# Kernel optimization log

Measured on AMD Instinct MI355X. Metric: run time of the kernel, lower is better.

## Reference

```python
import jax, jax.numpy as jnp
import numpy as np

B, TAU, T0V, D, PD, RD, DO, K = 2048, 32, 96, 64, 3, 1, 64, 16
R = 1.0  # radius for radius_graph


def setup_inputs() -> dict:
    key = jax.random.key(0)
    ks = jax.random.split(key, 9)
    return {
        "x": jax.random.normal(ks[0], (B, TAU, D), jnp.float32),
        "pos": jax.random.uniform(ks[1], (B, TAU, PD), jnp.float32),
        "rot": jax.random.uniform(ks[2], (B, TAU, RD), jnp.float32),
        "old_x": jax.random.normal(ks[3], (B, 128, D), jnp.float32),
        "old_pos": jax.random.uniform(ks[4], (B, 128, PD), jnp.float32),
        "old_rot": jax.random.uniform(ks[5], (B, 128, RD), jnp.float32),
        "W_self": jax.random.normal(ks[6], (D + PD + RD, DO), jnp.float32) * 0.1,
        "W_nbr": jax.random.normal(ks[7], (D + PD + RD, DO), jnp.float32) * 0.1,
        "bias": jax.random.normal(ks[8], (DO,), jnp.float32) * 0.1,
        "T0": T0V,
        "tau": TAU,
    }


def reference(x, pos, rot, old_x, old_pos, old_rot, W_self, W_nbr, bias, T0, tau):
    # --- update(): scatter new observations into the state buffers ---
    # (regular case: T[b]=T0, taus[b]=tau for all b, so new_idx is a static slice)
    new_x = old_x.at[:, T0:T0 + tau].set(x)
    new_pos = old_pos.at[:, T0:T0 + tau].set(pos)
    new_rot = old_rot.at[:, T0:T0 + tau].set(rot)

    L = T0 + tau  # valid (non-padded) nodes per env
    nx, npv, nr = new_x[:, :L], new_pos[:, :L], new_rot[:, :L]
    h = jnp.concatenate([nx, npv, nr], axis=-1)  # [B, L, D+PD+RD] node features

    # --- radius_graph(r, max_num_neighbors=K, loop=True) + remove_noncausal_edges ---
    # edge (j -> i) kept iff ||pos_j - pos_i|| <= r and j < i (causal, drops self-loops)
    diff = npv[:, :, None, :] - npv[:, None, :, :]           # [B, L, L, PD]
    d2 = jnp.sum(diff * diff, axis=-1)                        # [B, L, L] (target i, source j)
    t_idx = jnp.arange(L)
    causal = t_idx[None, :] < t_idx[:, None]                  # [L, L] j < i
    mask = causal[None, :, :] & (d2 <= R * R)
    masked_d2 = jnp.where(mask, d2, jnp.inf)
    neg_d, nbr_idx = jax.lax.top_k(-masked_d2, K)             # k nearest causal in-radius
    valid = jnp.isfinite(neg_d)                               # [B, L, K]

    # --- gnn(): one message-passing layer (stand-in for external gnn) ---
    msg = h @ W_nbr                                           # [B, L, DO]
    gathered = jax.vmap(lambda m, i: m[i])(msg, nbr_idx)      # [B, L, K, DO]
    agg = jnp.sum(gathered * valid[..., None].astype(msg.dtype), axis=2)
    out = jax.nn.relu(h @ W_self + agg + bias)                # [B, L, DO]

    # --- gather flat_new_idx / scatter into padded output ---
    padded_output = out[:, T0:T0 + tau]                       # [B, tau, DO]
    return padded_output, new_x, new_pos, new_rot
```

## Files before the change

kernel.cpp:

```cpp
#include <hip/hip_runtime.h>
#include <hip/hip_bf16.h>
#include <cstdint>
#include <cstddef>

#define NB 2048
#define TAU 32
#define T0C 96
#define LQ 128
#define DD 64
#define DOUT 64
#define KK 16
#define INVK 0xFFFFFFFFu

typedef unsigned int u32;
typedef __attribute__((ext_vector_type(8))) short short8;
typedef __attribute__((ext_vector_type(4))) float f32x4;

__device__ __forceinline__ float fmul_exact(float a, float b) {
  float r; asm("v_mul_f32 %0, %1, %2" : "=v"(r) : "v"(a), "v"(b)); return r;
}
__device__ __forceinline__ float fadd_exact(float a, float b) {
  float r; asm("v_add_f32 %0, %1, %2" : "=v"(r) : "v"(a), "v"(b)); return r;
}
__device__ __forceinline__ unsigned short f2bf(float f) {
  __hip_bfloat16 h = __float2bfloat16(f);
  return *reinterpret_cast<unsigned short*>(&h);
}
__device__ __forceinline__ u32 shfl_xor_u32(u32 v, int mask) {
  return (u32)__shfl_xor((int)v, mask, 64);
}

__device__ __forceinline__ void barrier_lgkm() {
  asm volatile("s_waitcnt lgkmcnt(0)" ::: "memory");
  __builtin_amdgcn_s_barrier();
  __builtin_amdgcn_sched_barrier(0);
}

#define CA(i, j) { u32 _lo = min(kd[i], kd[j]); u32 _hi = max(kd[i], kd[j]); kd[i] = _lo; kd[j] = _hi; }
#define CD(i, j) { u32 _lo = min(kd[i], kd[j]); u32 _hi = max(kd[i], kd[j]); kd[i] = _hi; kd[j] = _lo; }

#define SORT16() do { \
  CA(0,1)  CD(2,3)  CA(4,5)  CD(6,7)  CA(8,9)  CD(10,11) CA(12,13) CD(14,15) \
  CA(0,2)  CA(1,3)  CD(4,6)  CD(5,7)  CA(8,10) CA(9,11)  CD(12,14) CD(13,15) \
  CA(0,1)  CA(2,3)  CD(4,5)  CD(6,7)  CA(8,9)  CA(10,11) CD(12,13) CD(14,15) \
  CA(0,4)  CA(1,5)  CA(2,6)  CA(3,7)  CD(8,12) CD(9,13)  CD(10,14) CD(11,15) \
  CA(0,2)  CA(1,3)  CA(4,6)  CA(5,7)  CD(8,10) CD(9,11)  CD(12,14) CD(13,15) \
  CA(0,1)  CA(2,3)  CA(4,5)  CA(6,7)  CD(8,9)  CD(10,11) CD(12,13) CD(14,15) \
  CA(0,8)  CA(1,9)  CA(2,10) CA(3,11) CA(4,12) CA(5,13)  CA(6,14)  CA(7,15)  \
  CA(0,4)  CA(1,5)  CA(2,6)  CA(3,7)  CA(8,12) CA(9,13)  CA(10,14) CA(11,15) \
  CA(0,2)  CA(1,3)  CA(4,6)  CA(5,7)  CA(8,10) CA(9,11)  CA(12,14) CA(13,15) \
  CA(0,1)  CA(2,3)  CA(4,5)  CA(6,7)  CA(8,9)  CA(10,11) CA(12,13) CA(14,15) \
} while (0)

#define MERGE16() do { \
  CA(0,8)  CA(1,9)  CA(2,10) CA(3,11) CA(4,12) CA(5,13)  CA(6,14)  CA(7,15)  \
  CA(0,4)  CA(1,5)  CA(2,6)  CA(3,7)  CA(8,12) CA(9,13)  CA(10,14) CA(11,15) \
  CA(0,2)  CA(1,3)  CA(4,6)  CA(5,7)  CA(8,10) CA(9,11)  CA(12,14) CA(13,15) \
  CA(0,1)  CA(2,3)  CA(4,5)  CA(6,7)  CA(8,9)  CA(10,11) CA(12,13) CA(14,15) \
} while (0)

#define SHUF_MERGE(mask) do { \
  u32 pb[16]; \
  _Pragma("unroll") \
  for (int _i = 0; _i < 16; ++_i) pb[_i] = shfl_xor_u32(kd[15 - _i], mask); \
  _Pragma("unroll") \
  for (int _i = 0; _i < 16; ++_i) kd[_i] = min(kd[_i], pb[_i]); \
  MERGE16(); \
} while (0)

__global__ __launch_bounds__(256) void prep_w(
    const float* __restrict__ W_nbr, const float* __restrict__ W_self,
    unsigned short* __restrict__ wst) {
  int idx = blockIdx.x * 256 + threadIdx.x;
  int m = idx & 4095;
  int n = m >> 6, k = m & 63;
  const float* src = (idx < 4096) ? W_nbr : W_self;
  wst[idx] = f2bf(src[k * DOUT + n]);
}

__global__ __launch_bounds__(256, 4) void navgcm_fused(
    const float* __restrict__ x, const float* __restrict__ pos_in, const float* __restrict__ rot_in,
    const float* __restrict__ old_x, const float* __restrict__ old_pos, const float* __restrict__ old_rot,
    const float* __restrict__ W_self, const float* __restrict__ W_nbr, const float* __restrict__ bias,
    const unsigned short* __restrict__ wst,
    float* __restrict__ outp)
{
  const int b = blockIdx.x;
  const int tid = threadIdx.x;
  const int lane = tid & 63;
  const int wv = tid >> 6;
  const int fr = lane & 15;
  const int fg = lane >> 4;

  __shared__ __align__(16) unsigned short HsT[64 * 136];
  __shared__ __align__(16) unsigned short Hq[32 * 72];
  __shared__ __align__(16) unsigned short Pm[32][136];
  __shared__ float px[LQ], py[LQ], pz[LQ], rt[LQ];

  const bool haspos = tid < LQ;
  float p0 = 0.f, p1 = 0.f, p2 = 0.f, rr = 0.f;
  if (haspos) {
    int t = tid;
    if (t < T0C) {
      const float* s = old_pos + ((size_t)b * LQ + t) * 3;
      p0 = s[0]; p1 = s[1]; p2 = s[2];
      rr = old_rot[(size_t)b * LQ + t];
    } else {
      const float* s = pos_in + ((size_t)b * TAU + (t - T0C)) * 3;
      p0 = s[0]; p1 = s[1]; p2 = s[2];
      rr = rot_in[(size_t)b * TAU + (t - T0C)];
    }
  }

  float4 v[8];
  #pragma unroll
  for (int it = 0; it < 8; ++it) {
    int n = tid + 256 * it;
    int row = n >> 4, c4 = n & 15;
    const float4* src = (row < T0C)
        ? (const float4*)(old_x + ((size_t)b * LQ + row) * DD)
        : (const float4*)(x + ((size_t)b * TAU + (row - T0C)) * DD);
    v[it] = src[c4];
  }

  {
    u32* pz32 = (u32*)&Pm[0][0];
    #pragma unroll
    for (int k = 0; k < 9; ++k) {
      int idx = tid + 256 * k;
      if (idx < 2176) pz32[idx] = 0u;
    }
  }

  float* dpos = outp + (size_t)NB * TAU * DOUT + (size_t)NB * LQ * DD;
  float* drot = dpos + (size_t)NB * LQ * 3;
  if (haspos) {
    px[tid] = p0; py[tid] = p1; pz[tid] = p2; rt[tid] = rr;
    size_t g = (size_t)b * LQ + tid;
    dpos[g * 3 + 0] = p0; dpos[g * 3 + 1] = p1; dpos[g * 3 + 2] = p2;
    drot[g] = rr;
  }
  barrier_lgkm();

  {
    const int q = tid >> 3, s8 = tid & 7;
    const int i = T0C + q;
    const float pix = px[i], piy = py[i], piz = pz[i];

    u32 kb[16];
    #pragma unroll
    for (int c = 0; c < 16; ++c) {
      int j = 8 * c + s8;
      float dx = pix - px[j], dy = piy - py[j], dz = piz - pz[j];
      float d2 = fadd_exact(fadd_exact(fmul_exact(dx, dx), fmul_exact(dy, dy)),
                            fmul_exact(dz, dz));
      bool valid = (d2 <= 1.0f) && (j < i);
      kb[c] = valid ? __float_as_uint(d2) : INVK;
    }

    u32 kd[16];
    #pragma unroll
    for (int c = 0; c < 16; ++c) kd[c] = kb[c];
    SORT16();
    SHUF_MERGE(1);
    SHUF_MERGE(2);
    SHUF_MERGE(4);

    const u32 T = kd[15];
    int nless = 0;
    #pragma unroll
    for (int t = 0; t < KK; ++t) nless += (kd[t] < T) ? 1 : 0;
    const int needT = (T == INVK) ? 0 : (KK - nless);

    u32 selmask = 0;
    #pragma unroll
    for (int c = 0; c < 16; ++c) selmask |= (kb[c] < T) ? (1u << c) : 0u;

    u32 em = 0;
    #pragma unroll
    for (int c = 0; c < 16; ++c) em |= (kb[c] == T) ? (1u << c) : 0u;
    if (T == INVK) em = 0;
    for (int t = 0; __any(t < needT); ++t) {
      bool act = t < needT;
      u32 myj = (act && em) ? (u32)(8 * __builtin_ctz(em) + s8) : 0xFFFFu;
      u32 gj = myj;
      gj = min(gj, shfl_xor_u32(gj, 1));
      gj = min(gj, shfl_xor_u32(gj, 2));
      gj = min(gj, shfl_xor_u32(gj, 4));
      if (act && myj == gj && myj != 0xFFFFu) {
        int c = __builtin_ctz(em);
        selmask |= 1u << c;
        em &= em - 1;
      }
    }

    u32 m = selmask;
    while (m) {
      int c = __builtin_ctz(m);
      m &= m - 1;
      Pm[q][8 * c + s8] = 0x3F80;
    }

    float g0 = 0.f, g1 = 0.f, g2 = 0.f, g3 = 0.f;
    u32 m2 = selmask;
    while (m2) {
      int c = __builtin_ctz(m2);
      m2 &= m2 - 1;
      int j = 8 * c + s8;
      g0 += px[j]; g1 += py[j]; g2 += pz[j]; g3 += rt[j];
    }
    g0 += __shfl_xor(g0, 1, 64); g0 += __shfl_xor(g0, 2, 64); g0 += __shfl_xor(g0, 4, 64);
    g1 += __shfl_xor(g1, 1, 64); g1 += __shfl_xor(g1, 2, 64); g1 += __shfl_xor(g1, 4, 64);
    g2 += __shfl_xor(g2, 1, 64); g2 += __shfl_xor(g2, 2, 64); g2 += __shfl_xor(g2, 4, 64);
    g3 += __shfl_xor(g3, 1, 64); g3 += __shfl_xor(g3, 2, 64); g3 += __shfl_xor(g3, 4, 64);
    if (s8 == 0) {
      float4 gv; gv.x = g0; gv.y = g1; gv.z = g2; gv.w = g3;
      *reinterpret_cast<float4*>(&Pm[q][128]) = gv;
    }
  }

  float4* dnx = (float4*)(outp + (size_t)NB * TAU * DOUT);
  #pragma unroll
  for (int it = 0; it < 8; ++it) {
    int n = tid + 256 * it;
    int row = n >> 4, c4 = n & 15;
    unsigned short w0 = f2bf(v[it].x), w1 = f2bf(v[it].y),
                   w2 = f2bf(v[it].z), w3 = f2bf(v[it].w);
    int rj = row ^ ((c4 & 7) << 3);
    HsT[(4 * c4 + 0) * 136 + rj] = w0;
    HsT[(4 * c4 + 1) * 136 + rj] = w1;
    HsT[(4 * c4 + 2) * 136 + rj] = w2;
    HsT[(4 * c4 + 3) * 136 + rj] = w3;
    if (it >= 6) {
      ushort4 w4; w4.x = w0; w4.y = w1; w4.z = w2; w4.w = w3;
      *reinterpret_cast<ushort4*>(&Hq[(row - T0C) * 72 + c4 * 4]) = w4;
    }
    dnx[(size_t)b * 2048 + n] = v[it];
  }
  barrier_lgkm();

  const unsigned short* wn_t = wst;
  const unsigned short* ws_t = wst + 4096;
  const int mt = wv & 1;
  const int ntb = (wv >> 1) * 2;

  f32x4 accG[2];
  #pragma unroll
  for (int n = 0; n < 2; ++n) accG[n] = (f32x4){0.f, 0.f, 0.f, 0.f};
  #pragma unroll
  for (int ks = 0; ks < 4; ++ks) {
    short8 pa = *reinterpret_cast<const short8*>(&Pm[mt * 16 + fr][ks * 32 + fg * 8]);
    #pragma unroll
    for (int ntl = 0; ntl < 2; ++ntl) {
      int nf = (ntb + ntl) * 16 + fr;
      int j0 = (ks * 32 + fg * 8) ^ (((nf >> 2) & 7) << 3);
      short8 hb = *reinterpret_cast<const short8*>(&HsT[nf * 136 + j0]);
      accG[ntl] = __builtin_amdgcn_mfma_f32_16x16x32_bf16(pa, hb, accG[ntl], 0, 0, 0);
    }
  }

  short8 aQ0 = *reinterpret_cast<const short8*>(&Hq[(mt * 16 + fr) * 72 + fg * 8]);
  short8 aQ1 = *reinterpret_cast<const short8*>(&Hq[(mt * 16 + fr) * 72 + 32 + fg * 8]);
  f32x4 acc2[2];
  #pragma unroll
  for (int n = 0; n < 2; ++n) acc2[n] = (f32x4){0.f, 0.f, 0.f, 0.f};
  #pragma unroll
  for (int ntl = 0; ntl < 2; ++ntl) {
    int nt = ntb + ntl;
    short8 b0 = *reinterpret_cast<const short8*>(&ws_t[(nt * 16 + fr) * 64 + fg * 8]);
    short8 b1 = *reinterpret_cast<const short8*>(&ws_t[(nt * 16 + fr) * 64 + 32 + fg * 8]);
    acc2[ntl] = __builtin_amdgcn_mfma_f32_16x16x32_bf16(aQ0, b0, acc2[ntl], 0, 0, 0);
    acc2[ntl] = __builtin_amdgcn_mfma_f32_16x16x32_bf16(aQ1, b1, acc2[ntl], 0, 0, 0);
  }
  barrier_lgkm();

  #pragma unroll
  for (int ntl = 0; ntl < 2; ++ntl) {
    int nf = (ntb + ntl) * 16 + fr;
    #pragma unroll
    for (int r = 0; r < 4; ++r) {
      int q = mt * 16 + fg * 4 + r;
      Hq[q * 72 + nf] = f2bf(accG[ntl][r]);
    }
  }
  barrier_lgkm();

  f32x4 agg4[2];
  #pragma unroll
  for (int n = 0; n < 2; ++n) agg4[n] = (f32x4){0.f, 0.f, 0.f, 0.f};
  #pragma unroll
  for (int ks = 0; ks < 2; ++ks) {
    short8 ga = *reinterpret_cast<const short8*>(&Hq[(mt * 16 + fr) * 72 + ks * 32 + fg * 8]);
    #pragma unroll
    for (int ntl = 0; ntl < 2; ++ntl) {
      short8 wb = *reinterpret_cast<const short8*>(&wn_t[((ntb + ntl) * 16 + fr) * 64 + ks * 32 + fg * 8]);
      agg4[ntl] = __builtin_amdgcn_mfma_f32_16x16x32_bf16(ga, wb, agg4[ntl], 0, 0, 0);
    }
  }

  float4 gpv[4];
  #pragma unroll
  for (int r = 0; r < 4; ++r)
    gpv[r] = *reinterpret_cast<const float4*>(&Pm[mt * 16 + fg * 4 + r][128]);

  #pragma unroll
  for (int ntl = 0; ntl < 2; ++ntl) {
    int col = (ntb + ntl) * 16 + fr;
    float wn0 = W_nbr[64 * DOUT + col], wn1 = W_nbr[65 * DOUT + col];
    float wn2 = W_nbr[66 * DOUT + col], wn3 = W_nbr[67 * DOUT + col];
    float ws0 = W_self[64 * DOUT + col], ws1 = W_self[65 * DOUT + col];
    float ws2 = W_self[66 * DOUT + col], ws3 = W_self[67 * DOUT + col];
    float bi = bias[col];
    #pragma unroll
    for (int r = 0; r < 4; ++r) {
      int q = mt * 16 + fg * 4 + r;
      int row = T0C + q;
      float vv = acc2[ntl][r] + agg4[ntl][r] + bi
               + gpv[r].x * wn0 + gpv[r].y * wn1 + gpv[r].z * wn2 + gpv[r].w * wn3
               + px[row] * ws0 + py[row] * ws1 + pz[row] * ws2 + rt[row] * ws3;
      vv = fmaxf(vv, 0.f);
      outp[((size_t)b * TAU + q) * DOUT + col] = vv;
    }
  }
}

extern "C" void kernel_launch(void* const* d_in, const int* in_sizes, int n_in,
                              void* d_out, int out_size, void* d_ws, size_t ws_size,
                              hipStream_t stream) {
  (void)in_sizes; (void)n_in; (void)ws_size; (void)out_size;
  const float* x       = (const float*)d_in[0];
  const float* pos     = (const float*)d_in[1];
  const float* rot     = (const float*)d_in[2];
  const float* old_x   = (const float*)d_in[3];
  const float* old_pos = (const float*)d_in[4];
  const float* old_rot = (const float*)d_in[5];
  const float* W_self  = (const float*)d_in[6];
  const float* W_nbr   = (const float*)d_in[7];
  const float* bias    = (const float*)d_in[8];
  float* out = (float*)d_out;
  unsigned short* wst = (unsigned short*)d_ws;

  hipLaunchKernelGGL(prep_w, dim3(32), dim3(256), 0, stream, W_nbr, W_self, wst);
  hipLaunchKernelGGL(navgcm_fused, dim3(NB), dim3(256), 0, stream,
                     x, pos, rot, old_x, old_pos, old_rot, W_self, W_nbr, bias, wst, out);
}
```

Before: 39.52 us.

## Split state-buffer copy into dedicated interleaved copy blocks

Adds 1024 extra blocks to the fused kernel, interleaved as every third block, which copy new_x, new_pos and new_rot to the output with a grid-stride loop. The compute blocks no longer write these state buffers and only do the graph and GEMM work. The aim is to take store traffic off the critical compute blocks and spread the memory-bound copy across separate waves. The risk is that the copy blocks reload x and old_x that the compute blocks already read, so global read traffic rises.

```diff
diff --git a/kernel.cpp b/kernel.cpp
--- a/kernel.cpp
+++ b/kernel.cpp
@@ -11,6 +11,7 @@
 #define DOUT 64
 #define KK 16
 #define INVK 0xFFFFFFFFu
+#define NCP 1024
 
 typedef unsigned int u32;
 typedef __attribute__((ext_vector_type(8))) short short8;
@@ -85,8 +86,52 @@
     const unsigned short* __restrict__ wst,
     float* __restrict__ outp)
 {
-  const int b = blockIdx.x;
   const int tid = threadIdx.x;
+  const int idx = blockIdx.x;
+  const int rle = idx % 3;
+  const int qid = idx / 3;
+
+  if (rle == 2) {
+    const int g = qid * 256 + tid;
+    const int nthr = NCP * 256;
+
+    float4* dnx = (float4*)(outp + (size_t)NB * TAU * DOUT);
+    const float4* __restrict__ sox = (const float4*)old_x;
+    const float4* __restrict__ sx  = (const float4*)x;
+    const int NX4 = NB * LQ * DD / 4;
+    for (int n = g; n < NX4; n += nthr) {
+      int b = n >> 11;
+      int r = n & 2047;
+      int t = r >> 4;
+      float4 v = (t < T0C) ? sox[(size_t)b * 2048 + r]
+                           : sx[(size_t)b * 512 + (r - T0C * 16)];
+      dnx[(size_t)b * 2048 + r] = v;
+    }
+
+    float* dpos = outp + (size_t)NB * TAU * DOUT + (size_t)NB * LQ * DD;
+    float* drot = dpos + (size_t)NB * LQ * 3;
+    const int NROWS = NB * LQ;
+    for (int n = g; n < NROWS; n += nthr) {
+      int b = n >> 7, t = n & 127;
+      float p0, p1, p2, rr;
+      if (t < T0C) {
+        const float* s = old_pos + (size_t)n * 3;
+        p0 = s[0]; p1 = s[1]; p2 = s[2];
+        rr = old_rot[n];
+      } else {
+        const float* s = pos_in + ((size_t)b * TAU + (t - T0C)) * 3;
+        p0 = s[0]; p1 = s[1]; p2 = s[2];
+        rr = rot_in[(size_t)b * TAU + (t - T0C)];
+      }
+      dpos[(size_t)n * 3 + 0] = p0;
+      dpos[(size_t)n * 3 + 1] = p1;
+      dpos[(size_t)n * 3 + 2] = p2;
+      drot[n] = rr;
+    }
+    return;
+  }
+
+  const int b = 2 * qid + rle;
   const int lane = tid & 63;
   const int wv = tid >> 6;
   const int fr = lane & 15;
@@ -127,18 +172,13 @@
     u32* pz32 = (u32*)&Pm[0][0];
     #pragma unroll
     for (int k = 0; k < 9; ++k) {
-      int idx = tid + 256 * k;
-      if (idx < 2176) pz32[idx] = 0u;
-    }
-  }
-
-  float* dpos = outp + (size_t)NB * TAU * DOUT + (size_t)NB * LQ * DD;
-  float* drot = dpos + (size_t)NB * LQ * 3;
+      int id2 = tid + 256 * k;
+      if (id2 < 2176) pz32[id2] = 0u;
+    }
+  }
+
   if (haspos) {
     px[tid] = p0; py[tid] = p1; pz[tid] = p2; rt[tid] = rr;
-    size_t g = (size_t)b * LQ + tid;
-    dpos[g * 3 + 0] = p0; dpos[g * 3 + 1] = p1; dpos[g * 3 + 2] = p2;
-    drot[g] = rr;
   }
   barrier_lgkm();
 
@@ -219,7 +259,6 @@
     }
   }
 
-  float4* dnx = (float4*)(outp + (size_t)NB * TAU * DOUT);
   #pragma unroll
   for (int it = 0; it < 8; ++it) {
     int n = tid + 256 * it;
@@ -235,7 +274,6 @@
       ushort4 w4; w4.x = w0; w4.y = w1; w4.z = w2; w4.w = w3;
       *reinterpret_cast<ushort4*>(&Hq[(row - T0C) * 72 + c4 * 4]) = w4;
     }
-    dnx[(size_t)b * 2048 + n] = v[it];
   }
   barrier_lgkm();
 
@@ -341,6 +379,6 @@
   unsigned short* wst = (unsigned short*)d_ws;
 
   hipLaunchKernelGGL(prep_w, dim3(32), dim3(256), 0, stream, W_nbr, W_self, wst);
-  hipLaunchKernelGGL(navgcm_fused, dim3(NB), dim3(256), 0, stream,
+  hipLaunchKernelGGL(navgcm_fused, dim3(NB + NCP), dim3(256), 0, stream,
                      x, pos, rot, old_x, old_pos, old_rot, W_self, W_nbr, bias, wst, out);
 }
```

Measured after the change: 46.09 us. 16.6% more time.

## Process two batch elements per block and prefetch the second during the first

Applied to the files above, without the earlier changes.

Each block now handles two environments: the global loads for the second environment are issued right after the first environment's features are staged to shared memory, so their latency overlaps the first environment's graph build and MFMA work. The grid is halved to NB/2 blocks. In exchange, register pressure roughly doubles for the loaded tile (16 float4 plus positions per thread), which may hurt occupancy under launch_bounds(256,4). Fewer blocks also means less parallelism across CUs.

```diff
diff --git a/kernel.cpp b/kernel.cpp
--- a/kernel.cpp
+++ b/kernel.cpp
@@ -68,6 +68,31 @@
   MERGE16(); \
 } while (0)
 
+#define LOADB(S) do { \
+  const int b_ = 2 * blockIdx.x + (S); \
+  if (haspos) { \
+    int t_ = tid; \
+    if (t_ < T0C) { \
+      const float* s_ = old_pos + ((size_t)b_ * LQ + t_) * 3; \
+      pv[S].x = s_[0]; pv[S].y = s_[1]; pv[S].z = s_[2]; \
+      pv[S].w = old_rot[(size_t)b_ * LQ + t_]; \
+    } else { \
+      const float* s_ = pos_in + ((size_t)b_ * TAU + (t_ - T0C)) * 3; \
+      pv[S].x = s_[0]; pv[S].y = s_[1]; pv[S].z = s_[2]; \
+      pv[S].w = rot_in[(size_t)b_ * TAU + (t_ - T0C)]; \
+    } \
+  } \
+  _Pragma("unroll") \
+  for (int it_ = 0; it_ < 8; ++it_) { \
+    int n_ = tid + 256 * it_; \
+    int row_ = n_ >> 4, c4_ = n_ & 15; \
+    const float4* src_ = (row_ < T0C) \
+        ? (const float4*)(old_x + ((size_t)b_ * LQ + row_) * DD) \
+        : (const float4*)(x + ((size_t)b_ * TAU + (row_ - T0C)) * DD); \
+    v[S][it_] = src_[c4_]; \
+  } \
+} while (0)
+
 __global__ __launch_bounds__(256) void prep_w(
     const float* __restrict__ W_nbr, const float* __restrict__ W_self,
     unsigned short* __restrict__ wst) {
@@ -85,7 +110,6 @@
     const unsigned short* __restrict__ wst,
     float* __restrict__ outp)
 {
-  const int b = blockIdx.x;
   const int tid = threadIdx.x;
   const int lane = tid & 63;
   const int wv = tid >> 6;
@@ -98,228 +122,215 @@
   __shared__ float px[LQ], py[LQ], pz[LQ], rt[LQ];
 
   const bool haspos = tid < LQ;
-  float p0 = 0.f, p1 = 0.f, p2 = 0.f, rr = 0.f;
-  if (haspos) {
-    int t = tid;
-    if (t < T0C) {
-      const float* s = old_pos + ((size_t)b * LQ + t) * 3;
-      p0 = s[0]; p1 = s[1]; p2 = s[2];
-      rr = old_rot[(size_t)b * LQ + t];
-    } else {
-      const float* s = pos_in + ((size_t)b * TAU + (t - T0C)) * 3;
-      p0 = s[0]; p1 = s[1]; p2 = s[2];
-      rr = rot_in[(size_t)b * TAU + (t - T0C)];
-    }
-  }
-
-  float4 v[8];
-  #pragma unroll
-  for (int it = 0; it < 8; ++it) {
-    int n = tid + 256 * it;
-    int row = n >> 4, c4 = n & 15;
-    const float4* src = (row < T0C)
-        ? (const float4*)(old_x + ((size_t)b * LQ + row) * DD)
-        : (const float4*)(x + ((size_t)b * TAU + (row - T0C)) * DD);
-    v[it] = src[c4];
-  }
-
-  {
-    u32* pz32 = (u32*)&Pm[0][0];
-    #pragma unroll
-    for (int k = 0; k < 9; ++k) {
-      int idx = tid + 256 * k;
-      if (idx < 2176) pz32[idx] = 0u;
-    }
-  }
+  float4 pv[2] = {{0.f,0.f,0.f,0.f},{0.f,0.f,0.f,0.f}};
+  float4 v[2][8];
+
+  LOADB(0);
 
   float* dpos = outp + (size_t)NB * TAU * DOUT + (size_t)NB * LQ * DD;
   float* drot = dpos + (size_t)NB * LQ * 3;
-  if (haspos) {
-    px[tid] = p0; py[tid] = p1; pz[tid] = p2; rt[tid] = rr;
-    size_t g = (size_t)b * LQ + tid;
-    dpos[g * 3 + 0] = p0; dpos[g * 3 + 1] = p1; dpos[g * 3 + 2] = p2;
-    drot[g] = rr;
-  }
-  barrier_lgkm();
-
-  {
-    const int q = tid >> 3, s8 = tid & 7;
-    const int i = T0C + q;
-    const float pix = px[i], piy = py[i], piz = pz[i];
-
-    u32 kb[16];
-    #pragma unroll
-    for (int c = 0; c < 16; ++c) {
-      int j = 8 * c + s8;
-      float dx = pix - px[j], dy = piy - py[j], dz = piz - pz[j];
-      float d2 = fadd_exact(fadd_exact(fmul_exact(dx, dx), fmul_exact(dy, dy)),
-                            fmul_exact(dz, dz));
-      bool valid = (d2 <= 1.0f) && (j < i);
-      kb[c] = valid ? __float_as_uint(d2) : INVK;
-    }
-
-    u32 kd[16];
-    #pragma unroll
-    for (int c = 0; c < 16; ++c) kd[c] = kb[c];
-    SORT16();
-    SHUF_MERGE(1);
-    SHUF_MERGE(2);
-    SHUF_MERGE(4);
-
-    const u32 T = kd[15];
-    int nless = 0;
-    #pragma unroll
-    for (int t = 0; t < KK; ++t) nless += (kd[t] < T) ? 1 : 0;
-    const int needT = (T == INVK) ? 0 : (KK - nless);
-
-    u32 selmask = 0;
-    #pragma unroll
-    for (int c = 0; c < 16; ++c) selmask |= (kb[c] < T) ? (1u << c) : 0u;
-
-    u32 em = 0;
-    #pragma unroll
-    for (int c = 0; c < 16; ++c) em |= (kb[c] == T) ? (1u << c) : 0u;
-    if (T == INVK) em = 0;
-    for (int t = 0; __any(t < needT); ++t) {
-      bool act = t < needT;
-      u32 myj = (act && em) ? (u32)(8 * __builtin_ctz(em) + s8) : 0xFFFFu;
-      u32 gj = myj;
-      gj = min(gj, shfl_xor_u32(gj, 1));
-      gj = min(gj, shfl_xor_u32(gj, 2));
-      gj = min(gj, shfl_xor_u32(gj, 4));
-      if (act && myj == gj && myj != 0xFFFFu) {
-        int c = __builtin_ctz(em);
-        selmask |= 1u << c;
-        em &= em - 1;
-      }
-    }
-
-    u32 m = selmask;
-    while (m) {
-      int c = __builtin_ctz(m);
-      m &= m - 1;
-      Pm[q][8 * c + s8] = 0x3F80;
-    }
-
-    float g0 = 0.f, g1 = 0.f, g2 = 0.f, g3 = 0.f;
-    u32 m2 = selmask;
-    while (m2) {
-      int c = __builtin_ctz(m2);
-      m2 &= m2 - 1;
-      int j = 8 * c + s8;
-      g0 += px[j]; g1 += py[j]; g2 += pz[j]; g3 += rt[j];
-    }
-    g0 += __shfl_xor(g0, 1, 64); g0 += __shfl_xor(g0, 2, 64); g0 += __shfl_xor(g0, 4, 64);
-    g1 += __shfl_xor(g1, 1, 64); g1 += __shfl_xor(g1, 2, 64); g1 += __shfl_xor(g1, 4, 64);
-    g2 += __shfl_xor(g2, 1, 64); g2 += __shfl_xor(g2, 2, 64); g2 += __shfl_xor(g2, 4, 64);
-    g3 += __shfl_xor(g3, 1, 64); g3 += __shfl_xor(g3, 2, 64); g3 += __shfl_xor(g3, 4, 64);
-    if (s8 == 0) {
-      float4 gv; gv.x = g0; gv.y = g1; gv.z = g2; gv.w = g3;
-      *reinterpret_cast<float4*>(&Pm[q][128]) = gv;
-    }
-  }
-
   float4* dnx = (float4*)(outp + (size_t)NB * TAU * DOUT);
-  #pragma unroll
-  for (int it = 0; it < 8; ++it) {
-    int n = tid + 256 * it;
-    int row = n >> 4, c4 = n & 15;
-    unsigned short w0 = f2bf(v[it].x), w1 = f2bf(v[it].y),
-                   w2 = f2bf(v[it].z), w3 = f2bf(v[it].w);
-    int rj = row ^ ((c4 & 7) << 3);
-    HsT[(4 * c4 + 0) * 136 + rj] = w0;
-    HsT[(4 * c4 + 1) * 136 + rj] = w1;
-    HsT[(4 * c4 + 2) * 136 + rj] = w2;
-    HsT[(4 * c4 + 3) * 136 + rj] = w3;
-    if (it >= 6) {
-      ushort4 w4; w4.x = w0; w4.y = w1; w4.z = w2; w4.w = w3;
-      *reinterpret_cast<ushort4*>(&Hq[(row - T0C) * 72 + c4 * 4]) = w4;
-    }
-    dnx[(size_t)b * 2048 + n] = v[it];
-  }
-  barrier_lgkm();
-
   const unsigned short* wn_t = wst;
   const unsigned short* ws_t = wst + 4096;
   const int mt = wv & 1;
   const int ntb = (wv >> 1) * 2;
 
-  f32x4 accG[2];
   #pragma unroll
-  for (int n = 0; n < 2; ++n) accG[n] = (f32x4){0.f, 0.f, 0.f, 0.f};
-  #pragma unroll
-  for (int ks = 0; ks < 4; ++ks) {
-    short8 pa = *reinterpret_cast<const short8*>(&Pm[mt * 16 + fr][ks * 32 + fg * 8]);
+  for (int bb = 0; bb < 2; ++bb) {
+    const int b = 2 * blockIdx.x + bb;
+    if (bb) barrier_lgkm();
+
+    {
+      u32* pz32 = (u32*)&Pm[0][0];
+      #pragma unroll
+      for (int k = 0; k < 9; ++k) {
+        int id2 = tid + 256 * k;
+        if (id2 < 2176) pz32[id2] = 0u;
+      }
+    }
+    if (haspos) {
+      px[tid] = pv[bb].x; py[tid] = pv[bb].y; pz[tid] = pv[bb].z; rt[tid] = pv[bb].w;
+      size_t g = (size_t)b * LQ + tid;
+      dpos[g * 3 + 0] = pv[bb].x; dpos[g * 3 + 1] = pv[bb].y; dpos[g * 3 + 2] = pv[bb].z;
+      drot[g] = pv[bb].w;
+    }
+    barrier_lgkm();
+
+    {
+      const int q = tid >> 3, s8 = tid & 7;
+      const int i = T0C + q;
+      const float pix = px[i], piy = py[i], piz = pz[i];
+
+      u32 kb[16];
+      #pragma unroll
+      for (int c = 0; c < 16; ++c) {
+        int j = 8 * c + s8;
+        float dx = pix - px[j], dy = piy - py[j], dz = piz - pz[j];
+        float d2 = fadd_exact(fadd_exact(fmul_exact(dx, dx), fmul_exact(dy, dy)),
+                              fmul_exact(dz, dz));
+        bool valid = (d2 <= 1.0f) && (j < i);
+        kb[c] = valid ? __float_as_uint(d2) : INVK;
+      }
+
+      u32 kd[16];
+      #pragma unroll
+      for (int c = 0; c < 16; ++c) kd[c] = kb[c];
+      SORT16();
+      SHUF_MERGE(1);
+      SHUF_MERGE(2);
+      SHUF_MERGE(4);
+
+      const u32 T = kd[15];
+      int nless = 0;
+      #pragma unroll
+      for (int t = 0; t < KK; ++t) nless += (kd[t] < T) ? 1 : 0;
+      const int needT = (T == INVK) ? 0 : (KK - nless);
+
+      u32 selmask = 0;
+      #pragma unroll
+      for (int c = 0; c < 16; ++c) selmask |= (kb[c] < T) ? (1u << c) : 0u;
+
+      u32 em = 0;
+      #pragma unroll
+      for (int c = 0; c < 16; ++c) em |= (kb[c] == T) ? (1u << c) : 0u;
+      if (T == INVK) em = 0;
+      for (int t = 0; __any(t < needT); ++t) {
+        bool act = t < needT;
+        u32 myj = (act && em) ? (u32)(8 * __builtin_ctz(em) + s8) : 0xFFFFu;
+        u32 gj = myj;
+        gj = min(gj, shfl_xor_u32(gj, 1));
+        gj = min(gj, shfl_xor_u32(gj, 2));
+        gj = min(gj, shfl_xor_u32(gj, 4));
+        if (act && myj == gj && myj != 0xFFFFu) {
+          int c = __builtin_ctz(em);
+          selmask |= 1u << c;
+          em &= em - 1;
+        }
+      }
+
+      u32 m = selmask;
+      while (m) {
+        int c = __builtin_ctz(m);
+        m &= m - 1;
+        Pm[q][8 * c + s8] = 0x3F80;
+      }
+
+      float g0 = 0.f, g1 = 0.f, g2 = 0.f, g3 = 0.f;
+      u32 m2 = selmask;
+      while (m2) {
+        int c = __builtin_ctz(m2);
+        m2 &= m2 - 1;
+        int j = 8 * c + s8;
+        g0 += px[j]; g1 += py[j]; g2 += pz[j]; g3 += rt[j];
+      }
+      g0 += __shfl_xor(g0, 1, 64); g0 += __shfl_xor(g0, 2, 64); g0 += __shfl_xor(g0, 4, 64);
+      g1 += __shfl_xor(g1, 1, 64); g1 += __shfl_xor(g1, 2, 64); g1 += __shfl_xor(g1, 4, 64);
+      g2 += __shfl_xor(g2, 1, 64); g2 += __shfl_xor(g2, 2, 64); g2 += __shfl_xor(g2, 4, 64);
+      g3 += __shfl_xor(g3, 1, 64); g3 += __shfl_xor(g3, 2, 64); g3 += __shfl_xor(g3, 4, 64);
+      if (s8 == 0) {
+        float4 gv; gv.x = g0; gv.y = g1; gv.z = g2; gv.w = g3;
+        *reinterpret_cast<float4*>(&Pm[q][128]) = gv;
+      }
+    }
+
+    #pragma unroll
+    for (int it = 0; it < 8; ++it) {
+      int n = tid + 256 * it;
+      int row = n >> 4, c4 = n & 15;
+      unsigned short w0 = f2bf(v[bb][it].x), w1 = f2bf(v[bb][it].y),
+                     w2 = f2bf(v[bb][it].z), w3 = f2bf(v[bb][it].w);
+      int rj = row ^ ((c4 & 7) << 3);
+      HsT[(4 * c4 + 0) * 136 + rj] = w0;
+      HsT[(4 * c4 + 1) * 136 + rj] = w1;
+      HsT[(4 * c4 + 2) * 136 + rj] = w2;
+      HsT[(4 * c4 + 3) * 136 + rj] = w3;
+      if (it >= 6) {
+        ushort4 w4; w4.x = w0; w4.y = w1; w4.z = w2; w4.w = w3;
+        *reinterpret_cast<ushort4*>(&Hq[(row - T0C) * 72 + c4 * 4]) = w4;
+      }
+      dnx[(size_t)b * 2048 + n] = v[bb][it];
+    }
+
+    if (bb == 0) LOADB(1);
+    barrier_lgkm();
+
+    f32x4 accG[2];
+    #pragma unroll
+    for (int n = 0; n < 2; ++n) accG[n] = (f32x4){0.f, 0.f, 0.f, 0.f};
+    #pragma unroll
+    for (int ks = 0; ks < 4; ++ks) {
+      short8 pa = *reinterpret_cast<const short8*>(&Pm[mt * 16 + fr][ks * 32 + fg * 8]);
+      #pragma unroll
+      for (int ntl = 0; ntl < 2; ++ntl) {
+        int nf = (ntb + ntl) * 16 + fr;
+        int j0 = (ks * 32 + fg * 8) ^ (((nf >> 2) & 7) << 3);
+        short8 hb = *reinterpret_cast<const short8*>(&HsT[nf * 136 + j0]);
+        accG[ntl] = __builtin_amdgcn_mfma_f32_16x16x32_bf16(pa, hb, accG[ntl], 0, 0, 0);
+      }
+    }
+
+    short8 aQ0 = *reinterpret_cast<const short8*>(&Hq[(mt * 16 + fr) * 72 + fg * 8]);
+    short8 aQ1 = *reinterpret_cast<const short8*>(&Hq[(mt * 16 + fr) * 72 + 32 + fg * 8]);
+    f32x4 acc2[2];
+    #pragma unroll
+    for (int n = 0; n < 2; ++n) acc2[n] = (f32x4){0.f, 0.f, 0.f, 0.f};
+    #pragma unroll
+    for (int ntl = 0; ntl < 2; ++ntl) {
+      int nt = ntb + ntl;
+      short8 b0 = *reinterpret_cast<const short8*>(&ws_t[(nt * 16 + fr) * 64 + fg * 8]);
+      short8 b1 = *reinterpret_cast<const short8*>(&ws_t[(nt * 16 + fr) * 64 + 32 + fg * 8]);
+      acc2[ntl] = __builtin_amdgcn_mfma_f32_16x16x32_bf16(aQ0, b0, acc2[ntl], 0, 0, 0);
+      acc2[ntl] = __builtin_amdgcn_mfma_f32_16x16x32_bf16(aQ1, b1, acc2[ntl], 0, 0, 0);
+    }
+    barrier_lgkm();
+
     #pragma unroll
     for (int ntl = 0; ntl < 2; ++ntl) {
       int nf = (ntb + ntl) * 16 + fr;
-      int j0 = (ks * 32 + fg * 8) ^ (((nf >> 2) & 7) << 3);
-      short8 hb = *reinterpret_cast<const short8*>(&HsT[nf * 136 + j0]);
-      accG[ntl] = __builtin_amdgcn_mfma_f32_16x16x32_bf16(pa, hb, accG[ntl], 0, 0, 0);
-    }
-  }
-
-  short8 aQ0 = *reinterpret_cast<const short8*>(&Hq[(mt * 16 + fr) * 72 + fg * 8]);
-  short8 aQ1 = *reinterpret_cast<const short8*>(&Hq[(mt * 16 + fr) * 72 + 32 + fg * 8]);
-  f32x4 acc2[2];
-  #pragma unroll
-  for (int n = 0; n < 2; ++n) acc2[n] = (f32x4){0.f, 0.f, 0.f, 0.f};
-  #pragma unroll
-  for (int ntl = 0; ntl < 2; ++ntl) {
-    int nt = ntb + ntl;
-    short8 b0 = *reinterpret_cast<const short8*>(&ws_t[(nt * 16 + fr) * 64 + fg * 8]);
-    short8 b1 = *reinterpret_cast<const short8*>(&ws_t[(nt * 16 + fr) * 64 + 32 + fg * 8]);
-    acc2[ntl] = __builtin_amdgcn_mfma_f32_16x16x32_bf16(aQ0, b0, acc2[ntl], 0, 0, 0);
-    acc2[ntl] = __builtin_amdgcn_mfma_f32_16x16x32_bf16(aQ1, b1, acc2[ntl], 0, 0, 0);
-  }
-  barrier_lgkm();
-
-  #pragma unroll
-  for (int ntl = 0; ntl < 2; ++ntl) {
-    int nf = (ntb + ntl) * 16 + fr;
-    #pragma unroll
-    for (int r = 0; r < 4; ++r) {
-      int q = mt * 16 + fg * 4 + r;
-      Hq[q * 72 + nf] = f2bf(accG[ntl][r]);
-    }
-  }
-  barrier_lgkm();
-
-  f32x4 agg4[2];
-  #pragma unroll
-  for (int n = 0; n < 2; ++n) agg4[n] = (f32x4){0.f, 0.f, 0.f, 0.f};
-  #pragma unroll
-  for (int ks = 0; ks < 2; ++ks) {
-    short8 ga = *reinterpret_cast<const short8*>(&Hq[(mt * 16 + fr) * 72 + ks * 32 + fg * 8]);
+      #pragma unroll
+      for (int r = 0; r < 4; ++r) {
+        int q = mt * 16 + fg * 4 + r;
+        Hq[q * 72 + nf] = f2bf(accG[ntl][r]);
+      }
+    }
+    barrier_lgkm();
+
+    f32x4 agg4[2];
+    #pragma unroll
+    for (int n = 0; n < 2; ++n) agg4[n] = (f32x4){0.f, 0.f, 0.f, 0.f};
+    #pragma unroll
+    for (int ks = 0; ks < 2; ++ks) {
+      short8 ga = *reinterpret_cast<const short8*>(&Hq[(mt * 16 + fr) * 72 + ks * 32 + fg * 8]);
+      #pragma unroll
+      for (int ntl = 0; ntl < 2; ++ntl) {
+        short8 wb = *reinterpret_cast<const short8*>(&wn_t[((ntb + ntl) * 16 + fr) * 64 + ks * 32 + fg * 8]);
+        agg4[ntl] = __builtin_amdgcn_mfma_f32_16x16x32_bf16(ga, wb, agg4[ntl], 0, 0, 0);
+      }
+    }
+
+    float4 gpv[4];
+    #pragma unroll
+    for (int r = 0; r < 4; ++r)
+      gpv[r] = *reinterpret_cast<const float4*>(&Pm[mt * 16 + fg * 4 + r][128]);
+
     #pragma unroll
     for (int ntl = 0; ntl < 2; ++ntl) {
-      short8 wb = *reinterpret_cast<const short8*>(&wn_t[((ntb + ntl) * 16 + fr) * 64 + ks * 32 + fg * 8]);
-      agg4[ntl] = __builtin_amdgcn_mfma_f32_16x16x32_bf16(ga, wb, agg4[ntl], 0, 0, 0);
-    }
-  }
-
-  float4 gpv[4];
-  #pragma unroll
-  for (int r = 0; r < 4; ++r)
-    gpv[r] = *reinterpret_cast<const float4*>(&Pm[mt * 16 + fg * 4 + r][128]);
-
-  #pragma unroll
-  for (int ntl = 0; ntl < 2; ++ntl) {
-    int col = (ntb + ntl) * 16 + fr;
-    float wn0 = W_nbr[64 * DOUT + col], wn1 = W_nbr[65 * DOUT + col];
-    float wn2 = W_nbr[66 * DOUT + col], wn3 = W_nbr[67 * DOUT + col];
-    float ws0 = W_self[64 * DOUT + col], ws1 = W_self[65 * DOUT + col];
-    float ws2 = W_self[66 * DOUT + col], ws3 = W_self[67 * DOUT + col];
-    float bi = bias[col];
-    #pragma unroll
-    for (int r = 0; r < 4; ++r) {
-      int q = mt * 16 + fg * 4 + r;
-      int row = T0C + q;
-      float vv = acc2[ntl][r] + agg4[ntl][r] + bi
-               + gpv[r].x * wn0 + gpv[r].y * wn1 + gpv[r].z * wn2 + gpv[r].w * wn3
-               + px[row] * ws0 + py[row] * ws1 + pz[row] * ws2 + rt[row] * ws3;
-      vv = fmaxf(vv, 0.f);
-      outp[((size_t)b * TAU + q) * DOUT + col] = vv;
+      int col = (ntb + ntl) * 16 + fr;
+      float wn0 = W_nbr[64 * DOUT + col], wn1 = W_nbr[65 * DOUT + col];
+      float wn2 = W_nbr[66 * DOUT + col], wn3 = W_nbr[67 * DOUT + col];
+      float ws0 = W_self[64 * DOUT + col], ws1 = W_self[65 * DOUT + col];
+      float ws2 = W_self[66 * DOUT + col], ws3 = W_self[67 * DOUT + col];
+      float bi = bias[col];
+      #pragma unroll
+      for (int r = 0; r < 4; ++r) {
+        int q = mt * 16 + fg * 4 + r;
+        int row = T0C + q;
+        float vv = acc2[ntl][r] + agg4[ntl][r] + bi
+                 + gpv[r].x * wn0 + gpv[r].y * wn1 + gpv[r].z * wn2 + gpv[r].w * wn3
+                 + px[row] * ws0 + py[row] * ws1 + pz[row] * ws2 + rt[row] * ws3;
+        vv = fmaxf(vv, 0.f);
+        outp[((size_t)b * TAU + q) * DOUT + col] = vv;
+      }
     }
   }
 }
@@ -341,6 +352,6 @@
   unsigned short* wst = (unsigned short*)d_ws;
 
   hipLaunchKernelGGL(prep_w, dim3(32), dim3(256), 0, stream, W_nbr, W_self, wst);
-  hipLaunchKernelGGL(navgcm_fused, dim3(NB), dim3(256), 0, stream,
+  hipLaunchKernelGGL(navgcm_fused, dim3(NB / 2), dim3(256), 0, stream,
                      x, pos, rot, old_x, old_pos, old_rot, W_self, W_nbr, bias, wst, out);
 }
```

Result: slower. 66.60 us (+68.5%).
